# Optimization experiments

Measured on AMD Instinct MI355X. Metric: run time of the kernel, lower is better.

The kernel has to match this reference:

```python
import jax, jax.numpy as jnp
import numpy as np

N_NODES = 100000


def setup_inputs() -> dict:
    key = jax.random.key(0)
    ks = jax.random.split(key, 4)
    x = jax.random.normal(ks[0], (N_NODES, 64), dtype=jnp.float32)
    edge_index = jax.random.randint(ks[1], (2, 1600000), 0, N_NODES, dtype=jnp.int64)
    # Glorot-ish scaled weights
    W1 = jax.random.normal(ks[2], (64, 64), dtype=jnp.float32) * (1.0 / np.sqrt(64))
    b1 = jnp.zeros((64,), dtype=jnp.float32)
    W2 = jax.random.normal(ks[3], (64, 19), dtype=jnp.float32) * (1.0 / np.sqrt(64))
    b2 = jnp.zeros((19,), dtype=jnp.float32)
    return {"x": x, "edge_index": edge_index, "W1": W1, "b1": b1, "W2": W2, "b2": b2}


def _gcn_norm(edge_index, num_nodes, dtype):
    # PyG gcn_norm: add self-loops (fill_value=1, improved=False), then
    # norm = deg^-1/2[src] * deg^-1/2[dst] with deg computed over destination.
    loops = jnp.arange(num_nodes, dtype=edge_index.dtype)
    src = jnp.concatenate([edge_index[0], loops])
    dst = jnp.concatenate([edge_index[1], loops])
    deg = jax.ops.segment_sum(jnp.ones_like(dst, dtype=dtype), dst, num_segments=num_nodes)
    dinv = jax.lax.rsqrt(deg)  # deg >= 1 thanks to self-loops
    norm = dinv[src] * dinv[dst]  # [E + N]
    return src, dst, norm


def _gcn_conv(h, src, dst, norm, W, b, num_nodes):
    hw = h @ W                                  # dense transform [N, d_out]
    msg = norm[:, None] * hw[src]               # gather + edge scaling [E+N, d_out]
    out = jax.ops.segment_sum(msg, dst, num_segments=num_nodes)  # scatter-add
    return out + b


def reference(x, edge_index, W1, b1, W2, b2):
    n = x.shape[0]
    src, dst, norm = _gcn_norm(edge_index, n, x.dtype)
    h = jax.nn.relu(_gcn_conv(x, src, dst, norm, W1, b1, n))
    # dropout is identity in eval mode (training=False)
    return _gcn_conv(h, src, dst, norm, W2, b2, n)
```

## Files before the change

### kernel.cpp

```cpp
#include <hip/hip_runtime.h>

#define TPB 256
#define BSH 5
#define BNODES 32
#define CAP 1024
#define EPB 4096
#define NBMAX 3200


__global__ void k_hist1(const int* __restrict__ dst, int* __restrict__ hist,
                        int nb, int E) {
    __shared__ int sh[NBMAX];
    int tid = threadIdx.x, blk = blockIdx.x;
    for (int i = tid; i < nb; i += TPB) sh[i] = 0;
    __syncthreads();
    int e0 = blk * EPB;
    for (int i = tid; i < EPB; i += TPB) {
        int e = e0 + i;
        if (e < E) atomicAdd(&sh[dst[e] >> BSH], 1);
    }
    __syncthreads();
    int* hrow = hist + (size_t)blk * nb;
    for (int i = tid; i < nb; i += TPB) hrow[i] = sh[i];
}

__global__ void k_scanoff(const int* __restrict__ hist, int* __restrict__ offs,
                          int* __restrict__ bcnt, int nblk, int nb) {
    int t = blockIdx.x * TPB + threadIdx.x;
    int b = t >> 3, s = t & 7;
    if (b >= nb) return;
    int nps = (nblk + 7) >> 3;
    int sum = 0;
    for (int q = 0; q < nps; ++q) {
        int blk = q * 8 + s;
        if (blk < nblk) sum += hist[(size_t)blk * nb + b];
    }
    int v = sum;
#pragma unroll
    for (int o = 1; o < 8; o <<= 1) {
        int u = __shfl_up(v, o, 8);
        if (s >= o) v += u;
    }
    int total = __shfl(v, 7, 8);
    if (s == 0) bcnt[b] = total;
    int off = b * CAP + (v - sum);
    for (int q = 0; q < nps; ++q) {
        int blk = q * 8 + s;
        if (blk < nblk) {
            offs[(size_t)blk * nb + b] = off;
            off += hist[(size_t)blk * nb + b];
        }
    }
}

__global__ void k_scatter(const int* __restrict__ src, const int* __restrict__ dst,
                          const int* __restrict__ offs, unsigned* __restrict__ ebuf,
                          int nb, int E) {
    __shared__ int cur[NBMAX];
    int tid = threadIdx.x, blk = blockIdx.x;
    const int* orow = offs + (size_t)blk * nb;
    for (int i = tid; i < nb; i += TPB) cur[i] = orow[i];
    __syncthreads();
    int e0 = blk * EPB;
    for (int i = tid; i < EPB; i += TPB) {
        int e = e0 + i;
        if (e < E) {
            int d = dst[e];
            int pos = atomicAdd(&cur[d >> BSH], 1);
            ebuf[pos] = ((unsigned)src[e] << BSH) | (unsigned)(d & (BNODES - 1));
        }
    }
}

__global__ void k_bcsr(const int* __restrict__ bcnt, const unsigned* __restrict__ ebuf,
                       int* __restrict__ csr, int* __restrict__ node_beg,
                       int* __restrict__ degi, float* __restrict__ dinv, int nb, int n) {
    __shared__ unsigned se[4][CAP];
    __shared__ int scnt[4][BNODES];
    __shared__ int sexc[4][BNODES];
    __shared__ int srnk[4][BNODES];
    int wv = threadIdx.x >> 6, lane = threadIdx.x & 63;
    int b = blockIdx.x * 4 + wv;
    bool act = (b < nb);
    if (lane < BNODES) { scnt[wv][lane] = 0; srnk[wv][lane] = 0; }
    __syncthreads();
    int cnt = 0;
    if (act) {
        cnt = bcnt[b];
        if (cnt > CAP) cnt = CAP;
        const unsigned* p = &ebuf[(size_t)b * CAP];
        for (int k = lane; k < cnt; k += 64) {
            unsigned pk = p[k];
            se[wv][k] = pk;
            atomicAdd(&scnt[wv][pk & (BNODES - 1)], 1);
        }
    }
    __syncthreads();
    if (act && lane < BNODES) {
        int dg = scnt[wv][lane];
        int v = dg;
#pragma unroll
        for (int off = 1; off < BNODES; off <<= 1) {
            int t = __shfl_up(v, off, BNODES);
            if (lane >= off) v += t;
        }
        int excl = v - dg;
        sexc[wv][lane] = excl;
        int node = b * BNODES + lane;
        if (node < n) {
            degi[node] = dg;
            node_beg[node] = b * CAP + excl;
            dinv[node] = rsqrtf((float)dg + 1.0f);
        }
    }
    __syncthreads();
    if (act) {
        int* csrb = csr + (size_t)b * CAP;
        for (int k = lane; k < cnt; k += 64) {
            unsigned pk = se[wv][k];
            int dl = pk & (BNODES - 1);
            int r = atomicAdd(&srnk[wv][dl], 1);
            csrb[sexc[wv][dl] + r] = (int)(pk >> BSH);
        }
    }
}


__global__ void k_xw64v(const float* __restrict__ x, const float* __restrict__ W,
                        const float* __restrict__ dinv, _Float16* __restrict__ g, int n) {
    __shared__ float Ws[64 * 64];
    __shared__ float xsT[64 * 64];
    int tid = threadIdx.x;
    int row0 = blockIdx.x * 64;
    for (int i = tid; i < 1024; i += TPB)
        reinterpret_cast<float4*>(Ws)[i] = reinterpret_cast<const float4*>(W)[i];
    {
        int rl = tid >> 2, cq = (tid & 3) * 16;
        int row = row0 + rl;
#pragma unroll
        for (int j4 = 0; j4 < 4; ++j4) {
            float4 v = make_float4(0.f, 0.f, 0.f, 0.f);
            if (row < n) v = *reinterpret_cast<const float4*>(x + (size_t)row * 64 + cq + j4 * 4);
            xsT[(cq + j4 * 4 + 0) * 64 + rl] = v.x;
            xsT[(cq + j4 * 4 + 1) * 64 + rl] = v.y;
            xsT[(cq + j4 * 4 + 2) * 64 + rl] = v.z;
            xsT[(cq + j4 * 4 + 3) * 64 + rl] = v.w;
        }
    }
    __syncthreads();
    int c4 = (tid & 15) * 4, rq = (tid >> 4) * 4;
    float acc[4][4] = {};
#pragma unroll 4
    for (int k = 0; k < 64; ++k) {
        float4 wv = *reinterpret_cast<const float4*>(Ws + k * 64 + c4);
        float4 xv = *reinterpret_cast<const float4*>(xsT + k * 64 + rq);
        const float* wp = (const float*)&wv;
        const float* xp = (const float*)&xv;
#pragma unroll
        for (int i = 0; i < 4; ++i)
#pragma unroll
            for (int j = 0; j < 4; ++j) acc[i][j] += xp[i] * wp[j];
    }
#pragma unroll
    for (int i = 0; i < 4; ++i) {
        int row = row0 + rq + i;
        if (row < n) {
            float dv = dinv[row];
            _Float16 o[4];
#pragma unroll
            for (int j = 0; j < 4; ++j) o[j] = (_Float16)(dv * acc[i][j]);
            *reinterpret_cast<ushort4*>(g + (size_t)row * 64 + c4) =
                *reinterpret_cast<const ushort4*>(o);
        }
    }
}

__global__ void k_xw19v(const _Float16* __restrict__ h, const float* __restrict__ W,
                        const float* __restrict__ dinv, _Float16* __restrict__ g2p, int n) {
    __shared__ float Ws[64 * 32];
    __shared__ float xsT[64 * 32];
    int tid = threadIdx.x;
    int row0 = blockIdx.x * 32;
    for (int i = tid; i < 64 * 32; i += TPB) {
        int k = i >> 5, c = i & 31;
        Ws[i] = (c < 19) ? W[k * 19 + c] : 0.f;
    }
    {
        int rl = tid >> 3, sq = tid & 7;
        int row = row0 + rl;
        if (row < n) {
            uint4 v = *(reinterpret_cast<const uint4*>(h + (size_t)row * 64) + sq);
            const _Float16* f = (const _Float16*)&v;
#pragma unroll
            for (int j = 0; j < 8; ++j) xsT[(sq * 8 + j) * 32 + rl] = (float)f[j];
        } else {
#pragma unroll
            for (int j = 0; j < 8; ++j) xsT[(sq * 8 + j) * 32 + rl] = 0.f;
        }
    }
    __syncthreads();
    int c = tid & 31, rg = (tid >> 5) * 4;
    float acc[4] = {};
#pragma unroll 4
    for (int k = 0; k < 64; ++k) {
        float wv = Ws[k * 32 + c];
        float4 xv = *reinterpret_cast<const float4*>(xsT + k * 32 + rg);
        const float* xp = (const float*)&xv;
#pragma unroll
        for (int i = 0; i < 4; ++i) acc[i] += xp[i] * wv;
    }
#pragma unroll
    for (int i = 0; i < 4; ++i) {
        int row = row0 + rg + i;
        if (row < n)
            g2p[(size_t)row * 32 + c] = (c < 19) ? (_Float16)(dinv[row] * acc[i])
                                                 : (_Float16)0.f;
    }
}


__global__ void k_gather64(const int* __restrict__ node_beg, const int* __restrict__ degi,
                           const int* __restrict__ csr, const float* __restrict__ dinv,
                           const _Float16* __restrict__ g, const float* __restrict__ b1,
                           _Float16* __restrict__ h, int n) {
    int node = blockIdx.x * 4 + (threadIdx.x >> 6);
    if (node >= n) return;
    int lane = threadIdx.x & 63;
    int eidx = lane >> 3, fch = lane & 7;
    int beg = node_beg[node], cnt = degi[node];
    float acc[8];
#pragma unroll
    for (int j = 0; j < 8; ++j) acc[j] = 0.f;
    for (int base = 0; base < cnt; base += 8) {
        int k = base + eidx;
        if (k < cnt) {
            int row = csr[beg + k];
            uint4 v = *((const uint4*)(g + (size_t)row * 64) + fch);
            const _Float16* f = (const _Float16*)&v;
#pragma unroll
            for (int j = 0; j < 8; ++j) acc[j] += (float)f[j];
        }
    }
#pragma unroll
    for (int m = 8; m < 64; m <<= 1) {
#pragma unroll
        for (int j = 0; j < 8; ++j) acc[j] += __shfl_xor(acc[j], m);
    }
    if (eidx == 0) {
        uint4 v = *((const uint4*)(g + (size_t)node * 64) + fch);
        const _Float16* f = (const _Float16*)&v;
        float dv = dinv[node];
        _Float16 outv[8];
#pragma unroll
        for (int j = 0; j < 8; ++j) {
            float val = dv * (acc[j] + (float)f[j]) + b1[fch * 8 + j];
            outv[j] = (_Float16)fmaxf(val, 0.f);
        }
        *((uint4*)(h + (size_t)node * 64) + fch) = *(const uint4*)outv;
    }
}

__global__ void k_gath19(const int* __restrict__ node_beg, const int* __restrict__ degi,
                         const int* __restrict__ csr, const float* __restrict__ dinv,
                         const _Float16* __restrict__ g2p, const float* __restrict__ b2,
                         float* __restrict__ out, int n) {
    int node = blockIdx.x * 4 + (threadIdx.x >> 6);
    if (node >= n) return;
    int lane = threadIdx.x & 63;
    int eidx = lane >> 2, fq = lane & 3;
    int beg = node_beg[node], cnt = degi[node];
    float acc[8];
#pragma unroll
    for (int j = 0; j < 8; ++j) acc[j] = 0.f;
    for (int base = 0; base < cnt; base += 16) {
        int k = base + eidx;
        if (k < cnt) {
            int row = csr[beg + k];
            uint4 v = *((const uint4*)(g2p + (size_t)row * 32) + fq);
            const _Float16* f = (const _Float16*)&v;
#pragma unroll
            for (int j = 0; j < 8; ++j) acc[j] += (float)f[j];
        }
    }
    if (eidx == 0) {
        uint4 v = *((const uint4*)(g2p + (size_t)node * 32) + fq);
        const _Float16* f = (const _Float16*)&v;
#pragma unroll
        for (int j = 0; j < 8; ++j) acc[j] += (float)f[j];
    }
#pragma unroll
    for (int m = 4; m < 64; m <<= 1) {
#pragma unroll
        for (int j = 0; j < 8; ++j) acc[j] += __shfl_xor(acc[j], m);
    }
    if (eidx == 0) {
        float dv = dinv[node];
#pragma unroll
        for (int j = 0; j < 8; ++j) {
            int cc = fq * 8 + j;
            if (cc < 19) out[(size_t)node * 19 + cc] = dv * acc[j] + b2[cc];
        }
    }
}


extern "C" void kernel_launch(void* const* d_in, const int* in_sizes, int n_in,
                              void* d_out, int out_size, void* d_ws, size_t ws_size,
                              hipStream_t stream) {
    const float* x  = (const float*)d_in[0];
    const int*   ei = (const int*)d_in[1];
    const float* W1 = (const float*)d_in[2];
    const float* b1 = (const float*)d_in[3];
    const float* W2 = (const float*)d_in[4];
    const float* b2 = (const float*)d_in[5];
    float* out = (float*)d_out;

    int N = in_sizes[0] / 64;
    int E = in_sizes[1] / 2;
    const int* src = ei;
    const int* dst = ei + E;

    int NB = (N + BNODES - 1) >> BSH;
    int NBLK = (E + EPB - 1) / EPB;

    char* w = (char*)d_ws;
    int* bcnt      = (int*)w;      w += (size_t)NB * 4;
    int* degi      = (int*)w;      w += (size_t)N * 4;
    int* node_beg  = (int*)w;      w += (size_t)N * 4;
    float* dinv    = (float*)w;    w += (size_t)N * 4;
    w = (char*)(((size_t)w + 63) & ~(size_t)63);
    char* regionA  = w;
    size_t histB   = (size_t)NBLK * NB * 4;
    size_t csrB    = (size_t)NB * CAP * 4;
    size_t regA    = (histB * 2 > csrB) ? histB * 2 : csrB;
    int* hist      = (int*)regionA;
    int* offs      = (int*)(regionA + histB);
    int* csr       = (int*)regionA;
    w += regA;
    unsigned* ebuf = (unsigned*)w; w += (size_t)NB * CAP * 4;
    _Float16* g1   = (_Float16*)w; w += (size_t)N * 64 * 2;
    _Float16* h    = (_Float16*)w; w += (size_t)N * 64 * 2;
    _Float16* g2p  = g1;

    k_hist1   <<<NBLK, TPB, 0, stream>>>(dst, hist, NB, E);
    k_scanoff <<<(NB * 8 + TPB - 1) / TPB, TPB, 0, stream>>>(hist, offs, bcnt, NBLK, NB);
    k_scatter <<<NBLK, TPB, 0, stream>>>(src, dst, offs, ebuf, NB, E);
    k_bcsr    <<<(NB + 3) / 4, TPB, 0, stream>>>(bcnt, ebuf, csr, node_beg, degi, dinv, NB, N);

    k_xw64v   <<<(N + 63) / 64, TPB, 0, stream>>>(x, W1, dinv, g1, N);
    k_gather64<<<(N + 3) / 4, TPB, 0, stream>>>(node_beg, degi, csr, dinv, g1, b1, h, N);

    k_xw19v   <<<(N + 31) / 32, TPB, 0, stream>>>(h, W2, dinv, g2p, N);
    k_gath19  <<<(N + 3) / 4, TPB, 0, stream>>>(node_beg, degi, csr, dinv, g2p, b2, out, N);
}
```

Before: 223.9 us.

## Split layer-1 gather into feature halves and pack layer-2 features densely

The 64-feature aggregation now runs as two launches, each gathering one 32-feature half (64 bytes per row) with 16 edges per wavefront iteration, so each pass has a smaller working set of the fp16 feature table for cache reuse. The layer-2 transform now writes a dense 19-wide fp16 table instead of a 32-padded one, and the layer-2 gather uses one thread per output feature with 8 independent accumulators. This cuts the bytes moved in the second aggregation. The cost is reading the CSR index list twice in layer 1, and scalar 2-byte loads in layer 2.

```diff
diff --git a/kernel.cpp b/kernel.cpp
--- a/kernel.cpp
+++ b/kernel.cpp
@@ -176,7 +176,7 @@
 }
 
 __global__ void k_xw19v(const _Float16* __restrict__ h, const float* __restrict__ W,
-                        const float* __restrict__ dinv, _Float16* __restrict__ g2p, int n) {
+                        const float* __restrict__ dinv, _Float16* __restrict__ g2, int n) {
     __shared__ float Ws[64 * 32];
     __shared__ float xsT[64 * 32];
     int tid = threadIdx.x;
@@ -209,66 +209,27 @@
 #pragma unroll
         for (int i = 0; i < 4; ++i) acc[i] += xp[i] * wv;
     }
-#pragma unroll
-    for (int i = 0; i < 4; ++i) {
-        int row = row0 + rg + i;
-        if (row < n)
-            g2p[(size_t)row * 32 + c] = (c < 19) ? (_Float16)(dinv[row] * acc[i])
-                                                 : (_Float16)0.f;
-    }
-}
-
-
-__global__ void k_gather64(const int* __restrict__ node_beg, const int* __restrict__ degi,
-                           const int* __restrict__ csr, const float* __restrict__ dinv,
-                           const _Float16* __restrict__ g, const float* __restrict__ b1,
-                           _Float16* __restrict__ h, int n) {
+    if (c < 19) {
+#pragma unroll
+        for (int i = 0; i < 4; ++i) {
+            int row = row0 + rg + i;
+            if (row < n) g2[(size_t)row * 19 + c] = (_Float16)(dinv[row] * acc[i]);
+        }
+    }
+}
+
+
+__global__ void k_gath64h(const int* __restrict__ node_beg, const int* __restrict__ degi,
+                          const int* __restrict__ csr, const float* __restrict__ dinv,
+                          const _Float16* __restrict__ g, const float* __restrict__ b1,
+                          _Float16* __restrict__ h, int n, int halfsel) {
     int node = blockIdx.x * 4 + (threadIdx.x >> 6);
     if (node >= n) return;
     int lane = threadIdx.x & 63;
-    int eidx = lane >> 3, fch = lane & 7;
+    int eidx = lane >> 2, fch = lane & 3;
     int beg = node_beg[node], cnt = degi[node];
-    float acc[8];
-#pragma unroll
-    for (int j = 0; j < 8; ++j) acc[j] = 0.f;
-    for (int base = 0; base < cnt; base += 8) {
-        int k = base + eidx;
-        if (k < cnt) {
-            int row = csr[beg + k];
-            uint4 v = *((const uint4*)(g + (size_t)row * 64) + fch);
-            const _Float16* f = (const _Float16*)&v;
-#pragma unroll
-            for (int j = 0; j < 8; ++j) acc[j] += (float)f[j];
-        }
-    }
-#pragma unroll
-    for (int m = 8; m < 64; m <<= 1) {
-#pragma unroll
-        for (int j = 0; j < 8; ++j) acc[j] += __shfl_xor(acc[j], m);
-    }
-    if (eidx == 0) {
-        uint4 v = *((const uint4*)(g + (size_t)node * 64) + fch);
-        const _Float16* f = (const _Float16*)&v;
-        float dv = dinv[node];
-        _Float16 outv[8];
-#pragma unroll
-        for (int j = 0; j < 8; ++j) {
-            float val = dv * (acc[j] + (float)f[j]) + b1[fch * 8 + j];
-            outv[j] = (_Float16)fmaxf(val, 0.f);
-        }
-        *((uint4*)(h + (size_t)node * 64) + fch) = *(const uint4*)outv;
-    }
-}
-
-__global__ void k_gath19(const int* __restrict__ node_beg, const int* __restrict__ degi,
-                         const int* __restrict__ csr, const float* __restrict__ dinv,
-                         const _Float16* __restrict__ g2p, const float* __restrict__ b2,
-                         float* __restrict__ out, int n) {
-    int node = blockIdx.x * 4 + (threadIdx.x >> 6);
-    if (node >= n) return;
-    int lane = threadIdx.x & 63;
-    int eidx = lane >> 2, fq = lane & 3;
-    int beg = node_beg[node], cnt = degi[node];
+    const uint4* gb = (const uint4*)g;
+    int coff = halfsel * 4 + fch;
     float acc[8];
 #pragma unroll
     for (int j = 0; j < 8; ++j) acc[j] = 0.f;
@@ -276,31 +237,67 @@
         int k = base + eidx;
         if (k < cnt) {
             int row = csr[beg + k];
-            uint4 v = *((const uint4*)(g2p + (size_t)row * 32) + fq);
+            uint4 v = gb[(size_t)row * 8 + coff];
             const _Float16* f = (const _Float16*)&v;
 #pragma unroll
             for (int j = 0; j < 8; ++j) acc[j] += (float)f[j];
         }
     }
+#pragma unroll
+    for (int m = 4; m < 64; m <<= 1) {
+#pragma unroll
+        for (int j = 0; j < 8; ++j) acc[j] += __shfl_xor(acc[j], m);
+    }
     if (eidx == 0) {
-        uint4 v = *((const uint4*)(g2p + (size_t)node * 32) + fq);
+        uint4 v = gb[(size_t)node * 8 + coff];
         const _Float16* f = (const _Float16*)&v;
-#pragma unroll
-        for (int j = 0; j < 8; ++j) acc[j] += (float)f[j];
-    }
-#pragma unroll
-    for (int m = 4; m < 64; m <<= 1) {
-#pragma unroll
-        for (int j = 0; j < 8; ++j) acc[j] += __shfl_xor(acc[j], m);
-    }
-    if (eidx == 0) {
         float dv = dinv[node];
+        int c0 = halfsel * 32 + fch * 8;
+        _Float16 outv[8];
 #pragma unroll
         for (int j = 0; j < 8; ++j) {
-            int cc = fq * 8 + j;
-            if (cc < 19) out[(size_t)node * 19 + cc] = dv * acc[j] + b2[cc];
-        }
-    }
+            float val = dv * (acc[j] + (float)f[j]) + b1[c0 + j];
+            outv[j] = (_Float16)fmaxf(val, 0.f);
+        }
+        *reinterpret_cast<uint4*>(h + (size_t)node * 64 + c0) =
+            *reinterpret_cast<const uint4*>(outv);
+    }
+}
+
+__global__ void k_gath19(const int* __restrict__ node_beg, const int* __restrict__ degi,
+                         const int* __restrict__ csr, const float* __restrict__ dinv,
+                         const _Float16* __restrict__ g2, const float* __restrict__ b2,
+                         float* __restrict__ out, int n) {
+    int node = blockIdx.x * 8 + (threadIdx.x >> 5);
+    if (node >= n) return;
+    int c = threadIdx.x & 31;
+    if (c >= 19) return;
+    int beg = node_beg[node], cnt = degi[node];
+    float a0 = (float)g2[(size_t)node * 19 + c];
+    float a1 = 0.f, a2 = 0.f, a3 = 0.f;
+    float a4 = 0.f, a5 = 0.f, a6 = 0.f, a7 = 0.f;
+    int k = 0;
+    for (; k + 7 < cnt; k += 8) {
+        int s0 = csr[beg + k];
+        int s1 = csr[beg + k + 1];
+        int s2 = csr[beg + k + 2];
+        int s3 = csr[beg + k + 3];
+        int s4 = csr[beg + k + 4];
+        int s5 = csr[beg + k + 5];
+        int s6 = csr[beg + k + 6];
+        int s7 = csr[beg + k + 7];
+        a0 += (float)g2[(size_t)s0 * 19 + c];
+        a1 += (float)g2[(size_t)s1 * 19 + c];
+        a2 += (float)g2[(size_t)s2 * 19 + c];
+        a3 += (float)g2[(size_t)s3 * 19 + c];
+        a4 += (float)g2[(size_t)s4 * 19 + c];
+        a5 += (float)g2[(size_t)s5 * 19 + c];
+        a6 += (float)g2[(size_t)s6 * 19 + c];
+        a7 += (float)g2[(size_t)s7 * 19 + c];
+    }
+    for (; k < cnt; ++k) a1 += (float)g2[(size_t)csr[beg + k] * 19 + c];
+    float s = ((a0 + a1) + (a2 + a3)) + ((a4 + a5) + (a6 + a7));
+    out[(size_t)node * 19 + c] = dinv[node] * s + b2[c];
 }
 
 
@@ -340,7 +337,7 @@
     unsigned* ebuf = (unsigned*)w; w += (size_t)NB * CAP * 4;
     _Float16* g1   = (_Float16*)w; w += (size_t)N * 64 * 2;
     _Float16* h    = (_Float16*)w; w += (size_t)N * 64 * 2;
-    _Float16* g2p  = g1;
+    _Float16* g2   = g1;
 
     k_hist1   <<<NBLK, TPB, 0, stream>>>(dst, hist, NB, E);
     k_scanoff <<<(NB * 8 + TPB - 1) / TPB, TPB, 0, stream>>>(hist, offs, bcnt, NBLK, NB);
@@ -348,8 +345,9 @@
     k_bcsr    <<<(NB + 3) / 4, TPB, 0, stream>>>(bcnt, ebuf, csr, node_beg, degi, dinv, NB, N);
 
     k_xw64v   <<<(N + 63) / 64, TPB, 0, stream>>>(x, W1, dinv, g1, N);
-    k_gather64<<<(N + 3) / 4, TPB, 0, stream>>>(node_beg, degi, csr, dinv, g1, b1, h, N);
-
-    k_xw19v   <<<(N + 31) / 32, TPB, 0, stream>>>(h, W2, dinv, g2p, N);
-    k_gath19  <<<(N + 3) / 4, TPB, 0, stream>>>(node_beg, degi, csr, dinv, g2p, b2, out, N);
-}
+    k_gath64h <<<(N + 3) / 4, TPB, 0, stream>>>(node_beg, degi, csr, dinv, g1, b1, h, N, 0);
+    k_gath64h <<<(N + 3) / 4, TPB, 0, stream>>>(node_beg, degi, csr, dinv, g1, b1, h, N, 1);
+
+    k_xw19v   <<<(N + 31) / 32, TPB, 0, stream>>>(h, W2, dinv, g2, N);
+    k_gath19  <<<(N + 7) / 8, TPB, 0, stream>>>(node_beg, degi, csr, dinv, g2, b2, out, N);
+}
```

New measurement: 230.0 us. 2.7% more time.
